# Optimization experiments

Measured on AMD Instinct MI355X. Metric: run time of the kernel, lower is better.

## Reference

```python
import jax, jax.numpy as jnp
import numpy as np

# Dimensions
T, B, N, E = 16, 16, 1024, 16384   # seq len, graphs per step, nodes/graph, edges/graph
F_IN, MID, H = 128, 16, 256        # node features, GCN mid channels, hidden_dim
RATIO = 0.8
K = int(np.ceil(RATIO * N))        # SAGPooling keeps K=820 nodes per graph


def setup_inputs() -> dict:
    key = jax.random.key(0)
    ks = jax.random.split(key, 16)
    def p(k, shape, s=0.05):
        return jax.random.normal(k, shape, dtype=jnp.float32) * s
    return {
        "x": jax.random.normal(ks[0], (T, B, N, F_IN), dtype=jnp.float32),
        "edge_index": jax.random.randint(ks[1], (T, B, 2, E), 0, N, dtype=jnp.int32),
        "conv1_W": p(ks[2], (F_IN, MID)),
        "conv1_b": p(ks[3], (MID,)),
        "sag_Wl": p(ks[4], (MID, 1)),   # GraphConv lin_rel (neighbor aggregate)
        "sag_Wr": p(ks[5], (MID, 1)),   # GraphConv lin_root (self)
        "sag_b": p(ks[6], (1,)),
        "conv2_W": p(ks[7], (MID, H)),
        "conv2_b": p(ks[8], (H,)),
        "W_ih": p(ks[9], (4 * H, H)),   # LSTM gates in PyTorch order i,f,g,o
        "W_hh": p(ks[10], (4 * H, H)),
        "b_ih": p(ks[11], (4 * H,)),
        "b_hh": p(ks[12], (4 * H,)),
        "cls_W": p(ks[13], (H, 1)),
        "cls_b": p(ks[14], (1,)),
    }


def _gcn(x, src, dst, w, W, b, n):
    # GCNConv with self-loops: out_i = sum_j d_i^-1/2 d_j^-1/2 w_ij (x_j W) + d_i^-1 (x_i W) + b
    h = x @ W                                            # [n, out]
    deg = jnp.ones((n,), x.dtype).at[dst].add(w)         # +1 for self-loop weight
    dinv = jax.lax.rsqrt(deg)
    coef = dinv[src] * dinv[dst] * w                     # [e]
    out = jnp.zeros_like(h).at[dst].add(h[src] * coef[:, None])
    return out + h * (dinv * dinv)[:, None] + b


def _graph_embed(x, ei, conv1_W, conv1_b, sag_Wl, sag_Wr, sag_b, conv2_W, conv2_b):
    src, dst = ei[0], ei[1]
    w = jnp.ones((E,), x.dtype)
    # conv1 + relu
    h1 = jax.nn.relu(_gcn(x, src, dst, w, conv1_W, conv1_b, N))
    # SAGPooling score via GraphConv(16 -> 1): sum-aggregate neighbors + root
    agg = jnp.zeros_like(h1).at[dst].add(h1[src])
    score = (agg @ sag_Wl + h1 @ sag_Wr + sag_b)[:, 0]   # [N]
    sv, perm = jax.lax.top_k(score, K)                   # top-k nodes
    xp = h1[perm] * jnp.tanh(sv)[:, None]                # gate kept nodes
    # remap edges to kept-node ids; drop edges touching removed nodes via zero weight
    newidx = jnp.full((N,), -1, jnp.int32).at[perm].set(jnp.arange(K, dtype=jnp.int32))
    ns, nd = newidx[src], newidx[dst]
    valid = (ns >= 0) & (nd >= 0)
    ew = valid.astype(x.dtype)
    ns = jnp.where(valid, ns, 0)
    nd = jnp.where(valid, nd, 0)
    # conv2 + relu, then global mean pool over the K kept nodes
    h2 = jax.nn.relu(_gcn(xp, ns, nd, ew, conv2_W, conv2_b, K))
    return h2.mean(axis=0)                               # [H]


def reference(x, edge_index, conv1_W, conv1_b, sag_Wl, sag_Wr, sag_b,
              conv2_W, conv2_b, W_ih, W_hh, b_ih, b_hh, cls_W, cls_b):
    embed = lambda xg, eg: _graph_embed(xg, eg, conv1_W, conv1_b,
                                        sag_Wl, sag_Wr, sag_b, conv2_W, conv2_b)
    emb = jax.vmap(jax.vmap(embed))(x, edge_index)       # [T, B, H]

    def step(carry, xt):
        h, c = carry
        g = xt @ W_ih.T + b_ih + h @ W_hh.T + b_hh
        i, f, gg, o = jnp.split(g, 4, axis=-1)
        c = jax.nn.sigmoid(f) * c + jax.nn.sigmoid(i) * jnp.tanh(gg)
        h = jax.nn.sigmoid(o) * jnp.tanh(c)
        return (h, c), None

    h0 = jnp.zeros((B, H), x.dtype)
    (hT, _), _ = jax.lax.scan(step, (h0, h0), emb)       # hT = lstm_out[:, -1, :]
    return hT @ cls_W + cls_b                            # [B, 1]
```

## Files before the change

### kernel.cpp

```cpp
#include <hip/hip_runtime.h>
#include <cmath>

#define TT 16
#define BB 16
#define NN 1024
#define EE 16384
#define FIN 128
#define MIDC 16
#define HH 256
#define KK 820
#define HS 20

#define OFF_HBUF   0
#define N_HBUF     (NN*HS)
#define OFF_CSR    (OFF_HBUF + N_HBUF)
#define N_CSR      (EE/2)
#define OFF_HEAD   (OFF_CSR + N_CSR)
#define OFF_CUR    (OFF_HEAD + NN + 1)
#define OFF_SCANA  (OFF_CUR + NN)
#define OFF_DINV   (OFF_SCANA + NN)
#define OFF_UB     (OFF_DINV + NN)
#define OFF_HIST   (OFF_UB + NN)
#define OFF_S      (OFF_HIST + 256)
#define OFF_WCNT   (OFF_S + 256)
#define OFF_CTRL   (OFF_WCNT + 16)
#define SM_FLOATS  (OFF_CTRL + 8)
#define SM_BYTES   (SM_FLOATS * 4)

__global__ __launch_bounds__(1024) void k_graph(
    const float* __restrict__ x, const int* __restrict__ ei,
    const float* __restrict__ W1, const float* __restrict__ b1,
    const float* __restrict__ Wl, const float* __restrict__ Wr,
    const float* __restrict__ bsag, const float* __restrict__ W2,
    const float* __restrict__ b2, float* __restrict__ emb)
{
  extern __shared__ __align__(16) float sm[];
  float*          hbuf  = sm + OFF_HBUF;
  float4*         hb4   = (float4*)hbuf;
  unsigned short* csr   = (unsigned short*)(sm + OFF_CSR);
  int*            head  = (int*)(sm + OFF_HEAD);
  int*            cur   = (int*)(sm + OFF_CUR);
  int*            scanA = (int*)(sm + OFF_SCANA);
  int*            scanB = (int*)(sm + OFF_DINV);
  float*          dinvb = sm + OFF_DINV;
  unsigned*       ubv   = (unsigned*)(sm + OFF_UB);
  int*            hist  = (int*)(sm + OFF_HIST);
  int*            S     = (int*)(sm + OFF_S);
  int*            wcnt  = (int*)(sm + OFF_WCNT);
  int*            ctrl  = (int*)(sm + OFF_CTRL);

  const int g   = blockIdx.x;
  const int tid = threadIdx.x;
  const float* xg   = x  + (size_t)g * (NN*FIN);
  const int*   srcp = ei + (size_t)g * (2*EE);
  const int*   dstp = srcp + EE;

  cur[tid] = 0;

  float hown[MIDC];
  {
    const float4* xr = (const float4*)(xg + (size_t)tid * FIN);
#pragma unroll
    for (int c = 0; c < MIDC; ++c) hown[c] = 0.0f;
    for (int k4 = 0; k4 < FIN/4; ++k4) {
      float4 v = xr[k4];
      const float* w0 = W1 + (k4*4 + 0)*MIDC;
      const float* w1 = W1 + (k4*4 + 1)*MIDC;
      const float* w2 = W1 + (k4*4 + 2)*MIDC;
      const float* w3 = W1 + (k4*4 + 3)*MIDC;
#pragma unroll
      for (int c = 0; c < MIDC; ++c)
        hown[c] += v.x*w0[c] + v.y*w1[c] + v.z*w2[c] + v.w*w3[c];
    }
    hb4[tid*5+0] = make_float4(hown[0],  hown[1],  hown[2],  hown[3]);
    hb4[tid*5+1] = make_float4(hown[4],  hown[5],  hown[6],  hown[7]);
    hb4[tid*5+2] = make_float4(hown[8],  hown[9],  hown[10], hown[11]);
    hb4[tid*5+3] = make_float4(hown[12], hown[13], hown[14], hown[15]);
  }
  __syncthreads();

  for (int e = tid; e < EE; e += 1024) atomicAdd(&cur[dstp[e]], 1);
  __syncthreads();

  {
    int v = cur[tid];
    scanA[tid] = v;
    __syncthreads();
    int* s_ = scanA; int* d_ = scanB;
    for (int off = 1; off < NN; off <<= 1) {
      int t = s_[tid];
      if (tid >= off) t += s_[tid - off];
      d_[tid] = t;
      __syncthreads();
      int* tmp = s_; s_ = d_; d_ = tmp;
    }
    int inc = s_[tid];
    int ex  = inc - v;
    __syncthreads();
    head[tid] = ex;
    cur[tid]  = ex;
    if (tid == 0) head[NN] = EE;
    dinvb[tid] = rsqrtf((float)(v + 1));
  }
  __syncthreads();

  for (int e = tid; e < EE; e += 1024) {
    int s = srcp[e], d = dstp[e];
    int pos = atomicAdd(&cur[d], 1);
    csr[pos] = (unsigned short)s;
  }
  __syncthreads();

  const int beg = head[tid], end = head[tid+1];

  float h1own[MIDC];
  {
    float accv[MIDC];
#pragma unroll
    for (int c = 0; c < MIDC; ++c) accv[c] = 0.0f;
    for (int p = beg; p < end; ++p) {
      int s = csr[p];
      float ds_ = dinvb[s];
      float4 a0 = hb4[s*5+0], a1 = hb4[s*5+1], a2 = hb4[s*5+2], a3 = hb4[s*5+3];
      accv[0]  += a0.x*ds_; accv[1]  += a0.y*ds_; accv[2]  += a0.z*ds_; accv[3]  += a0.w*ds_;
      accv[4]  += a1.x*ds_; accv[5]  += a1.y*ds_; accv[6]  += a1.z*ds_; accv[7]  += a1.w*ds_;
      accv[8]  += a2.x*ds_; accv[9]  += a2.y*ds_; accv[10] += a2.z*ds_; accv[11] += a2.w*ds_;
      accv[12] += a3.x*ds_; accv[13] += a3.y*ds_; accv[14] += a3.z*ds_; accv[15] += a3.w*ds_;
    }
    float di = dinvb[tid];
#pragma unroll
    for (int c = 0; c < MIDC; ++c)
      h1own[c] = fmaxf(di*accv[c] + hown[c]*di*di + b1[c], 0.0f);
  }
  __syncthreads();
  hb4[tid*5+0] = make_float4(h1own[0],  h1own[1],  h1own[2],  h1own[3]);
  hb4[tid*5+1] = make_float4(h1own[4],  h1own[5],  h1own[6],  h1own[7]);
  hb4[tid*5+2] = make_float4(h1own[8],  h1own[9],  h1own[10], h1own[11]);
  hb4[tid*5+3] = make_float4(h1own[12], h1own[13], h1own[14], h1own[15]);
  __syncthreads();

  float score;
  unsigned myu;
  {
    float aggv[MIDC];
#pragma unroll
    for (int c = 0; c < MIDC; ++c) aggv[c] = 0.0f;
    for (int p = beg; p < end; ++p) {
      int s = csr[p];
      float4 a0 = hb4[s*5+0], a1 = hb4[s*5+1], a2 = hb4[s*5+2], a3 = hb4[s*5+3];
      aggv[0]  += a0.x; aggv[1]  += a0.y; aggv[2]  += a0.z; aggv[3]  += a0.w;
      aggv[4]  += a1.x; aggv[5]  += a1.y; aggv[6]  += a1.z; aggv[7]  += a1.w;
      aggv[8]  += a2.x; aggv[9]  += a2.y; aggv[10] += a2.z; aggv[11] += a2.w;
      aggv[12] += a3.x; aggv[13] += a3.y; aggv[14] += a3.z; aggv[15] += a3.w;
    }
    score = bsag[0];
#pragma unroll
    for (int c = 0; c < MIDC; ++c) score += aggv[c]*Wl[c] + h1own[c]*Wr[c];
    unsigned ubits = __float_as_uint(score);
    myu = (ubits & 0x80000000u) ? ~ubits : (ubits | 0x80000000u);
  }

  int remK = KK;
  unsigned pref = 0;
  for (int byte = 3; byte >= 0; --byte) {
    if (tid < 256) hist[tid] = 0;
    __syncthreads();
    const int sh = byte * 8;
    const unsigned hi_mask = (byte == 3) ? 0u : (0xFFFFFFFFu << (sh + 8));
    if ((myu & hi_mask) == pref) atomicAdd(&hist[(myu >> sh) & 255u], 1);
    __syncthreads();
    if (tid < 64) {
      int h0 = hist[tid*4+0], h1_ = hist[tid*4+1], h2_ = hist[tid*4+2], h3_ = hist[tid*4+3];
      int s3 = h3_, s2 = h2_ + s3, s1 = h1_ + s2, s0 = h0 + s1;
      int run = s0;
#pragma unroll
      for (int off = 1; off < 64; off <<= 1) {
        int o = __shfl_down(run, off);
        if (tid + off < 64) run += o;
      }
      int above = run - s0;
      S[tid*4+0] = above + s0;
      S[tid*4+1] = above + s1;
      S[tid*4+2] = above + s2;
      S[tid*4+3] = above + s3;
    }
    __syncthreads();
    if (tid < 256) {
      int Sv = S[tid];
      int Sn = (tid < 255) ? S[tid+1] : 0;
      if (Sv >= remK && Sn < remK) { ctrl[0] = remK - Sn; ctrl[1] = tid; }
    }
    __syncthreads();
    remK  = ctrl[0];
    pref |= ((unsigned)ctrl[1]) << sh;
    __syncthreads();
  }
  const unsigned vstar = pref;
  const int need = remK;

  {
    const int wid = tid >> 6, lane = tid & 63;
    bool eq = (myu == vstar);
    unsigned long long m = __ballot(eq);
    if (lane == 0) wcnt[wid] = __popcll(m);
    __syncthreads();
    int before = (lane == 0) ? 0 : __popcll(m & ((~0ull) >> (64 - lane)));
    for (int w = 0; w < wid; ++w) before += wcnt[w];
    int kept = (myu > vstar) ? 1 : (eq ? (before < need) : 0);
    float gate = kept ? tanhf(score) : 0.0f;
#pragma unroll
    for (int c = 0; c < MIDC; ++c) h1own[c] *= gate;
    hb4[tid*5+0] = make_float4(h1own[0],  h1own[1],  h1own[2],  h1own[3]);
    hb4[tid*5+1] = make_float4(h1own[4],  h1own[5],  h1own[6],  h1own[7]);
    hb4[tid*5+2] = make_float4(h1own[8],  h1own[9],  h1own[10], h1own[11]);
    hb4[tid*5+3] = make_float4(h1own[12], h1own[13], h1own[14], h1own[15]);
    ubv[tid] = (unsigned)kept;
  }
  __syncthreads();

  float di2;
  {
    int cnt2 = 0;
    for (int p = beg; p < end; ++p) cnt2 += (int)ubv[csr[p]];
    di2 = rsqrtf((float)(1 + cnt2));
    dinvb[tid] = di2;
  }
  __syncthreads();

  {
    float acc2[MIDC];
#pragma unroll
    for (int c = 0; c < MIDC; ++c) acc2[c] = 0.0f;
    for (int p = beg; p < end; ++p) {
      int s = csr[p];
      float ds_ = dinvb[s];
      float4 a0 = hb4[s*5+0], a1 = hb4[s*5+1], a2 = hb4[s*5+2], a3 = hb4[s*5+3];
      acc2[0]  += a0.x*ds_; acc2[1]  += a0.y*ds_; acc2[2]  += a0.z*ds_; acc2[3]  += a0.w*ds_;
      acc2[4]  += a1.x*ds_; acc2[5]  += a1.y*ds_; acc2[6]  += a1.z*ds_; acc2[7]  += a1.w*ds_;
      acc2[8]  += a2.x*ds_; acc2[9]  += a2.y*ds_; acc2[10] += a2.z*ds_; acc2[11] += a2.w*ds_;
      acc2[12] += a3.x*ds_; acc2[13] += a3.y*ds_; acc2[14] += a3.z*ds_; acc2[15] += a3.w*ds_;
    }
#pragma unroll
    for (int c = 0; c < MIDC; ++c)
      h1own[c] = di2*acc2[c] + h1own[c]*di2*di2;
  }
  __syncthreads();
  hb4[tid*5+0] = make_float4(h1own[0],  h1own[1],  h1own[2],  h1own[3]);
  hb4[tid*5+1] = make_float4(h1own[4],  h1own[5],  h1own[6],  h1own[7]);
  hb4[tid*5+2] = make_float4(h1own[8],  h1own[9],  h1own[10], h1own[11]);
  hb4[tid*5+3] = make_float4(h1own[12], h1own[13], h1own[14], h1own[15]);
  __syncthreads();

  {
    const int ig = tid >> 6, h4 = tid & 63;
    float4 w2c[MIDC];
#pragma unroll
    for (int c = 0; c < MIDC; ++c) w2c[c] = *(const float4*)(W2 + c*HH + (h4 << 2));
    float4 bv = *(const float4*)(b2 + (h4 << 2));
    float4 pacc = make_float4(0.f, 0.f, 0.f, 0.f);
    for (int k = 0; k < 64; ++k) {
      int i = (ig << 6) + k;
      if (ubv[i] == 0u) continue;
      float4 v0 = hb4[i*5+0], v1 = hb4[i*5+1], v2 = hb4[i*5+2], v3 = hb4[i*5+3];
      float vv[MIDC] = {v0.x,v0.y,v0.z,v0.w, v1.x,v1.y,v1.z,v1.w,
                        v2.x,v2.y,v2.z,v2.w, v3.x,v3.y,v3.z,v3.w};
      float t0 = bv.x, t1 = bv.y, t2 = bv.z, t3 = bv.w;
#pragma unroll
      for (int c = 0; c < MIDC; ++c) {
        t0 += vv[c]*w2c[c].x; t1 += vv[c]*w2c[c].y;
        t2 += vv[c]*w2c[c].z; t3 += vv[c]*w2c[c].w;
      }
      pacc.x += fmaxf(t0, 0.f); pacc.y += fmaxf(t1, 0.f);
      pacc.z += fmaxf(t2, 0.f); pacc.w += fmaxf(t3, 0.f);
    }
    float4* part4 = (float4*)(sm + OFF_CSR);
    part4[(ig << 6) + h4] = pacc;
  }
  __syncthreads();
  if (tid < HH) {
    const float* part = sm + OFF_CSR;
    float s = 0.f;
#pragma unroll
    for (int ig = 0; ig < 16; ++ig) s += part[ig*HH + tid];
    emb[(size_t)g*HH + tid] = s * (1.0f/(float)KK);
  }
}

__global__ __launch_bounds__(1024) void k_gatepre(
    const float* __restrict__ emb, const float* __restrict__ W_ih,
    const float* __restrict__ b_ih, const float* __restrict__ b_hh,
    float* __restrict__ A)
{
  __shared__ __align__(16) float es[HH];
  const int g = blockIdx.x, tid = threadIdx.x;
  const int wid = tid >> 6, lane = tid & 63;
  const int sub = lane & 15, rq = lane >> 4;
  if (tid < HH) es[tid] = emb[(size_t)g*HH + tid];
  __syncthreads();
  const float4* e4 = (const float4*)es;
  for (int it = 0; it < 16; ++it) {
    const int j = it*64 + wid*4 + rq;
    const float4* wr = (const float4*)(W_ih + (size_t)j*HH);
    float p = 0.f;
#pragma unroll
    for (int kk = 0; kk < 4; ++kk) {
      float4 w = wr[sub + 16*kk];
      float4 e = e4[sub + 16*kk];
      p += w.x*e.x + w.y*e.y + w.z*e.z + w.w*e.w;
    }
    p += __shfl_xor(p, 1); p += __shfl_xor(p, 2);
    p += __shfl_xor(p, 4); p += __shfl_xor(p, 8);
    if (sub == 0) A[(size_t)g*1024 + j] = p + b_ih[j] + b_hh[j];
  }
}

__global__ __launch_bounds__(256) void k_step(
    const float* __restrict__ A_t, const float* __restrict__ W_hh,
    const float* __restrict__ h_in, float* __restrict__ h_out,
    float* __restrict__ cbuf)
{
  __shared__ __align__(16) float hsh[HH];
  __shared__ float gl[16][4];
  const int b = blockIdx.x >> 4, ug = blockIdx.x & 15;
  const int tid = threadIdx.x;
  const int ul = tid >> 4, sub = tid & 15;
  if (tid < HH) hsh[tid] = h_in[b*HH + tid];
  __syncthreads();
  const float4* h4 = (const float4*)hsh;
  float4 hv0 = h4[sub], hv1 = h4[sub+16], hv2 = h4[sub+32], hv3 = h4[sub+48];
  const int u = ug*16 + ul;
  float gv[4];
#pragma unroll
  for (int gg_ = 0; gg_ < 4; ++gg_) {
    const float4* wr = (const float4*)(W_hh + (size_t)(gg_*HH + u)*HH);
    float4 w0 = wr[sub], w1 = wr[sub+16], w2 = wr[sub+32], w3 = wr[sub+48];
    float p = w0.x*hv0.x + w0.y*hv0.y + w0.z*hv0.z + w0.w*hv0.w
            + w1.x*hv1.x + w1.y*hv1.y + w1.z*hv1.z + w1.w*hv1.w
            + w2.x*hv2.x + w2.y*hv2.y + w2.z*hv2.z + w2.w*hv2.w
            + w3.x*hv3.x + w3.y*hv3.y + w3.z*hv3.z + w3.w*hv3.w;
    p += __shfl_xor(p, 1); p += __shfl_xor(p, 2);
    p += __shfl_xor(p, 4); p += __shfl_xor(p, 8);
    gv[gg_] = p;
  }
  if (sub == 0) { gl[ul][0]=gv[0]; gl[ul][1]=gv[1]; gl[ul][2]=gv[2]; gl[ul][3]=gv[3]; }
  __syncthreads();
  if (tid < 16) {
    const int uu = ug*16 + tid;
    const float* At = A_t + b*1024;
    float gi = gl[tid][0] + At[uu      ];
    float gf = gl[tid][1] + At[uu + 256];
    float gn = gl[tid][2] + At[uu + 512];
    float go = gl[tid][3] + At[uu + 768];
    float iv = 1.0f/(1.0f + expf(-gi));
    float fv = 1.0f/(1.0f + expf(-gf));
    float gvv = tanhf(gn);
    float ov = 1.0f/(1.0f + expf(-go));
    float c = fv * cbuf[b*HH + uu] + iv * gvv;
    cbuf[b*HH + uu] = c;
    h_out[b*HH + uu] = ov * tanhf(c);
  }
}

__global__ __launch_bounds__(256) void k_cls(
    const float* __restrict__ h, const float* __restrict__ cls_W,
    const float* __restrict__ cls_b, float* __restrict__ out)
{
  __shared__ float red[4];
  const int b = blockIdx.x, tid = threadIdx.x;
  float p = h[b*HH + tid] * cls_W[tid];
#pragma unroll
  for (int off = 32; off >= 1; off >>= 1) p += __shfl_down(p, off);
  if ((tid & 63) == 0) red[tid >> 6] = p;
  __syncthreads();
  if (tid == 0) out[b] = red[0] + red[1] + red[2] + red[3] + cls_b[0];
}

extern "C" void kernel_launch(void* const* d_in, const int* in_sizes, int n_in,
                              void* d_out, int out_size, void* d_ws, size_t ws_size,
                              hipStream_t stream)
{
  const float* x    = (const float*)d_in[0];
  const int*   ei   = (const int*)  d_in[1];
  const float* W1   = (const float*)d_in[2];
  const float* b1   = (const float*)d_in[3];
  const float* Wl   = (const float*)d_in[4];
  const float* Wr   = (const float*)d_in[5];
  const float* bs   = (const float*)d_in[6];
  const float* W2   = (const float*)d_in[7];
  const float* b2   = (const float*)d_in[8];
  const float* Wih  = (const float*)d_in[9];
  const float* Whh  = (const float*)d_in[10];
  const float* bih  = (const float*)d_in[11];
  const float* bhh  = (const float*)d_in[12];
  const float* clsW = (const float*)d_in[13];
  const float* clsb = (const float*)d_in[14];
  float* out = (float*)d_out;

  float* emb = (float*)d_ws;
  float* A   = emb + (size_t)TT*BB*HH;
  float* hA  = emb;
  float* hB  = emb + BB*HH;
  float* cb  = emb + 2*BB*HH;

  (void)hipFuncSetAttribute(reinterpret_cast<const void*>(k_graph),
      hipFuncAttributeMaxDynamicSharedMemorySize, SM_BYTES);

  hipLaunchKernelGGL(k_graph, dim3(TT*BB), dim3(1024), SM_BYTES, stream,
                     x, ei, W1, b1, Wl, Wr, bs, W2, b2, emb);
  hipLaunchKernelGGL(k_gatepre, dim3(TT*BB), dim3(1024), 0, stream,
                     emb, Wih, bih, bhh, A);
  (void)hipMemsetAsync(hA, 0, BB*HH*sizeof(float), stream);
  (void)hipMemsetAsync(cb, 0, BB*HH*sizeof(float), stream);
  for (int t = 0; t < TT; ++t) {
    const float* hin  = (t & 1) ? hB : hA;
    float*       hout = (t & 1) ? hA : hB;
    hipLaunchKernelGGL(k_step, dim3(256), dim3(256), 0, stream,
                       A + (size_t)t*BB*1024, Whh, hin, hout, cb);
  }
  hipLaunchKernelGGL(k_cls, dim3(BB), dim3(256), 0, stream, hA, clsW, clsb, out);
}
```

Before: 423.6 us.

## Fuse LSTM gate precompute, recurrent steps and classifier into one persistent kernel

```diff
diff --git a/kernel.cpp b/kernel.cpp
--- a/kernel.cpp
+++ b/kernel.cpp
@@ -286,93 +286,121 @@
   }
 }
 
-__global__ __launch_bounds__(1024) void k_gatepre(
+__global__ __launch_bounds__(256) void k_lstm(
     const float* __restrict__ emb, const float* __restrict__ W_ih,
-    const float* __restrict__ b_ih, const float* __restrict__ b_hh,
-    float* __restrict__ A)
+    const float* __restrict__ W_hh, const float* __restrict__ b_ih,
+    const float* __restrict__ b_hh, const float* __restrict__ clsW,
+    const float* __restrict__ clsb, float* __restrict__ hA,
+    float* __restrict__ hB, int* __restrict__ bar, float* __restrict__ out)
 {
-  __shared__ __align__(16) float es[HH];
-  const int g = blockIdx.x, tid = threadIdx.x;
-  const int wid = tid >> 6, lane = tid & 63;
-  const int sub = lane & 15, rq = lane >> 4;
-  if (tid < HH) es[tid] = emb[(size_t)g*HH + tid];
-  __syncthreads();
-  const float4* e4 = (const float4*)es;
-  for (int it = 0; it < 16; ++it) {
-    const int j = it*64 + wid*4 + rq;
+  __shared__ __align__(16) float emb_s[16][HH];
+  __shared__ __align__(16) float A_s[16][64];
+  __shared__ __align__(16) float h_s[HH];
+  __shared__ float gl[16][4];
+
+  const int bid = blockIdx.x;
+  const int b   = bid & 15, ug = bid >> 4;
+  const int tid = threadIdx.x;
+  const int ul  = tid >> 4, sub = tid & 15;
+  const int u   = ug*16 + ul;
+
+  for (int i = tid; i < 16*HH; i += 256) {
+    int t = i >> 8, k = i & 255;
+    emb_s[t][k] = emb[(size_t)(t*BB + b)*HH + k];
+  }
+
+  float4 wh[4][4];
+#pragma unroll
+  for (int g_ = 0; g_ < 4; ++g_) {
+    const float4* wr = (const float4*)(W_hh + (size_t)(g_*HH + u)*HH);
+    wh[g_][0] = wr[sub];      wh[g_][1] = wr[sub+16];
+    wh[g_][2] = wr[sub+32];   wh[g_][3] = wr[sub+48];
+  }
+  __syncthreads();
+
+#pragma unroll
+  for (int g_ = 0; g_ < 4; ++g_) {
+    const int j = g_*HH + u;
     const float4* wr = (const float4*)(W_ih + (size_t)j*HH);
-    float p = 0.f;
-#pragma unroll
-    for (int kk = 0; kk < 4; ++kk) {
-      float4 w = wr[sub + 16*kk];
-      float4 e = e4[sub + 16*kk];
-      p += w.x*e.x + w.y*e.y + w.z*e.z + w.w*e.w;
-    }
-    p += __shfl_xor(p, 1); p += __shfl_xor(p, 2);
-    p += __shfl_xor(p, 4); p += __shfl_xor(p, 8);
-    if (sub == 0) A[(size_t)g*1024 + j] = p + b_ih[j] + b_hh[j];
-  }
-}
-
-__global__ __launch_bounds__(256) void k_step(
-    const float* __restrict__ A_t, const float* __restrict__ W_hh,
-    const float* __restrict__ h_in, float* __restrict__ h_out,
-    float* __restrict__ cbuf)
-{
-  __shared__ __align__(16) float hsh[HH];
-  __shared__ float gl[16][4];
-  const int b = blockIdx.x >> 4, ug = blockIdx.x & 15;
-  const int tid = threadIdx.x;
-  const int ul = tid >> 4, sub = tid & 15;
-  if (tid < HH) hsh[tid] = h_in[b*HH + tid];
-  __syncthreads();
-  const float4* h4 = (const float4*)hsh;
-  float4 hv0 = h4[sub], hv1 = h4[sub+16], hv2 = h4[sub+32], hv3 = h4[sub+48];
-  const int u = ug*16 + ul;
-  float gv[4];
-#pragma unroll
-  for (int gg_ = 0; gg_ < 4; ++gg_) {
-    const float4* wr = (const float4*)(W_hh + (size_t)(gg_*HH + u)*HH);
     float4 w0 = wr[sub], w1 = wr[sub+16], w2 = wr[sub+32], w3 = wr[sub+48];
-    float p = w0.x*hv0.x + w0.y*hv0.y + w0.z*hv0.z + w0.w*hv0.w
-            + w1.x*hv1.x + w1.y*hv1.y + w1.z*hv1.z + w1.w*hv1.w
-            + w2.x*hv2.x + w2.y*hv2.y + w2.z*hv2.z + w2.w*hv2.w
-            + w3.x*hv3.x + w3.y*hv3.y + w3.z*hv3.z + w3.w*hv3.w;
-    p += __shfl_xor(p, 1); p += __shfl_xor(p, 2);
-    p += __shfl_xor(p, 4); p += __shfl_xor(p, 8);
-    gv[gg_] = p;
-  }
-  if (sub == 0) { gl[ul][0]=gv[0]; gl[ul][1]=gv[1]; gl[ul][2]=gv[2]; gl[ul][3]=gv[3]; }
-  __syncthreads();
-  if (tid < 16) {
-    const int uu = ug*16 + tid;
-    const float* At = A_t + b*1024;
-    float gi = gl[tid][0] + At[uu      ];
-    float gf = gl[tid][1] + At[uu + 256];
-    float gn = gl[tid][2] + At[uu + 512];
-    float go = gl[tid][3] + At[uu + 768];
-    float iv = 1.0f/(1.0f + expf(-gi));
-    float fv = 1.0f/(1.0f + expf(-gf));
-    float gvv = tanhf(gn);
-    float ov = 1.0f/(1.0f + expf(-go));
-    float c = fv * cbuf[b*HH + uu] + iv * gvv;
-    cbuf[b*HH + uu] = c;
-    h_out[b*HH + uu] = ov * tanhf(c);
-  }
-}
-
-__global__ __launch_bounds__(256) void k_cls(
-    const float* __restrict__ h, const float* __restrict__ cls_W,
-    const float* __restrict__ cls_b, float* __restrict__ out)
-{
-  __shared__ float red[4];
-  const int b = blockIdx.x, tid = threadIdx.x;
-  float p = h[b*HH + tid] * cls_W[tid];
-#pragma unroll
-  for (int off = 32; off >= 1; off >>= 1) p += __shfl_down(p, off);
-  if ((tid & 63) == 0) red[tid >> 6] = p;
-  __syncthreads();
-  if (tid == 0) out[b] = red[0] + red[1] + red[2] + red[3] + cls_b[0];
+    float bj = b_ih[j] + b_hh[j];
+    for (int t = 0; t < 16; ++t) {
+      const float4* e4 = (const float4*)emb_s[t];
+      float4 e0 = e4[sub], e1 = e4[sub+16], e2 = e4[sub+32], e3 = e4[sub+48];
+      float p = w0.x*e0.x + w0.y*e0.y + w0.z*e0.z + w0.w*e0.w
+              + w1.x*e1.x + w1.y*e1.y + w1.z*e1.z + w1.w*e1.w
+              + w2.x*e2.x + w2.y*e2.y + w2.z*e2.z + w2.w*e2.w
+              + w3.x*e3.x + w3.y*e3.y + w3.z*e3.z + w3.w*e3.w;
+      p += __shfl_xor(p, 1); p += __shfl_xor(p, 2);
+      p += __shfl_xor(p, 4); p += __shfl_xor(p, 8);
+      if (sub == 0) A_s[t][g_*16 + ul] = p + bj;
+    }
+  }
+  __syncthreads();
+
+  float c = 0.0f;
+  for (int s = 0; s < 16; ++s) {
+    if (s == 0) {
+      h_s[tid] = 0.0f;
+    } else {
+      const float* hr = (s & 1) ? hA : hB;
+      h_s[tid] = __hip_atomic_load(&hr[b*HH + tid], __ATOMIC_RELAXED,
+                                   __HIP_MEMORY_SCOPE_AGENT);
+    }
+    __syncthreads();
+
+    const float4* h4 = (const float4*)h_s;
+    float4 hv0 = h4[sub], hv1 = h4[sub+16], hv2 = h4[sub+32], hv3 = h4[sub+48];
+    float gv[4];
+#pragma unroll
+    for (int g_ = 0; g_ < 4; ++g_) {
+      float p = wh[g_][0].x*hv0.x + wh[g_][0].y*hv0.y + wh[g_][0].z*hv0.z + wh[g_][0].w*hv0.w
+              + wh[g_][1].x*hv1.x + wh[g_][1].y*hv1.y + wh[g_][1].z*hv1.z + wh[g_][1].w*hv1.w
+              + wh[g_][2].x*hv2.x + wh[g_][2].y*hv2.y + wh[g_][2].z*hv2.z + wh[g_][2].w*hv2.w
+              + wh[g_][3].x*hv3.x + wh[g_][3].y*hv3.y + wh[g_][3].z*hv3.z + wh[g_][3].w*hv3.w;
+      p += __shfl_xor(p, 1); p += __shfl_xor(p, 2);
+      p += __shfl_xor(p, 4); p += __shfl_xor(p, 8);
+      gv[g_] = p;
+    }
+    if (sub == 0) { gl[ul][0]=gv[0]; gl[ul][1]=gv[1]; gl[ul][2]=gv[2]; gl[ul][3]=gv[3]; }
+    __syncthreads();
+
+    if (tid < 16) {
+      float gi = gl[tid][0] + A_s[s][     tid];
+      float gf = gl[tid][1] + A_s[s][16 + tid];
+      float gn = gl[tid][2] + A_s[s][32 + tid];
+      float go = gl[tid][3] + A_s[s][48 + tid];
+      float iv = 1.0f/(1.0f + expf(-gi));
+      float fv = 1.0f/(1.0f + expf(-gf));
+      float gg = tanhf(gn);
+      float ov = 1.0f/(1.0f + expf(-go));
+      c = fv*c + iv*gg;
+      float hv = ov * tanhf(c);
+      float* hw = (s & 1) ? hB : hA;
+      __hip_atomic_store(&hw[b*HH + ug*16 + tid], hv, __ATOMIC_RELAXED,
+                         __HIP_MEMORY_SCOPE_AGENT);
+      if (s == 15) {
+        float p = hv * clsW[ug*16 + tid];
+        p += __shfl_xor(p, 1); p += __shfl_xor(p, 2);
+        p += __shfl_xor(p, 4); p += __shfl_xor(p, 8);
+        if (tid == 0) atomicAdd(&out[b], p + (ug == 0 ? clsb[0] : 0.0f));
+      }
+    }
+
+    if (s < 15) {
+      __syncthreads();
+      if (tid == 0) {
+        __threadfence();
+        atomicAdd(&bar[b], 1);
+        const int target = 16 * (s + 1);
+        while (__hip_atomic_load(&bar[b], __ATOMIC_RELAXED,
+                                 __HIP_MEMORY_SCOPE_AGENT) < target)
+          __builtin_amdgcn_s_sleep(4);
+        __threadfence();
+      }
+      __syncthreads();
+    }
+  }
 }
 
 extern "C" void kernel_launch(void* const* d_in, const int* in_sizes, int n_in,
@@ -397,25 +425,17 @@
   float* out = (float*)d_out;
 
   float* emb = (float*)d_ws;
-  float* A   = emb + (size_t)TT*BB*HH;
-  float* hA  = emb;
-  float* hB  = emb + BB*HH;
-  float* cb  = emb + 2*BB*HH;
+  float* hA  = emb + (size_t)TT*BB*HH;
+  float* hB  = hA + BB*HH;
+  int*   bar = (int*)(hB + BB*HH);
 
   (void)hipFuncSetAttribute(reinterpret_cast<const void*>(k_graph),
       hipFuncAttributeMaxDynamicSharedMemorySize, SM_BYTES);
 
   hipLaunchKernelGGL(k_graph, dim3(TT*BB), dim3(1024), SM_BYTES, stream,
                      x, ei, W1, b1, Wl, Wr, bs, W2, b2, emb);
-  hipLaunchKernelGGL(k_gatepre, dim3(TT*BB), dim3(1024), 0, stream,
-                     emb, Wih, bih, bhh, A);
-  (void)hipMemsetAsync(hA, 0, BB*HH*sizeof(float), stream);
-  (void)hipMemsetAsync(cb, 0, BB*HH*sizeof(float), stream);
-  for (int t = 0; t < TT; ++t) {
-    const float* hin  = (t & 1) ? hB : hA;
-    float*       hout = (t & 1) ? hA : hB;
-    hipLaunchKernelGGL(k_step, dim3(256), dim3(256), 0, stream,
-                       A + (size_t)t*BB*1024, Whh, hin, hout, cb);
-  }
-  hipLaunchKernelGGL(k_cls, dim3(BB), dim3(256), 0, stream, hA, clsW, clsb, out);
+  (void)hipMemsetAsync(bar, 0, BB*sizeof(int), stream);
+  (void)hipMemsetAsync(out, 0, BB*sizeof(float), stream);
+  hipLaunchKernelGGL(k_lstm, dim3(256), dim3(256), 0, stream,
+                     emb, Wih, Whh, bih, bhh, clsW, clsb, hA, hB, bar, out);
 }
```

Result: slower. 618.5 us (+46.0%).
